# Kernel optimization log

Measured on AMD Instinct MI355X. Metric: run time of the kernel, lower is better.

The kernel has to match this reference:

```python
import jax, jax.numpy as jnp
import numpy as np

MASK_ATTENTION = 10000000000.0
PAD_IDX = 0


def setup_inputs() -> dict:
    key = jax.random.key(0)
    ks = jax.random.split(key, 12)
    S, T, B, H, V = 256, 64, 8, 768, 50257
    return {
        "encoder_out": jax.random.normal(ks[0], (S, B, H), dtype=jnp.float32),
        "decoder_state": jax.random.normal(ks[1], (T, B, H), dtype=jnp.float32),
        "src_ids": jax.random.randint(ks[2], (S, B), 0, V, dtype=jnp.int64),
        "tgt_embedding": jax.random.normal(ks[3], (T, B, H), dtype=jnp.float32),
        "W_attn": jax.random.normal(ks[4], (2 * H, H), dtype=jnp.float32) * 0.02,
        "b_attn": jax.random.normal(ks[5], (H,), dtype=jnp.float32) * 0.02,
        "v_attn": jax.random.normal(ks[6], (H,), dtype=jnp.float32) * 0.02,
        "b_v": jax.random.normal(ks[7], (1,), dtype=jnp.float32) * 0.02,
        "W_pgen": jax.random.normal(ks[8], (3 * H, 1), dtype=jnp.float32) * 0.02,
        "b_pgen": jax.random.normal(ks[9], (1,), dtype=jnp.float32) * 0.02,
        "W_gen": jax.random.normal(ks[10], (H, V), dtype=jnp.float32) * 0.02,
        "b_gen": jax.random.normal(ks[11], (V,), dtype=jnp.float32) * 0.02,
    }


def reference(encoder_out, decoder_state, src_ids, tgt_embedding,
              W_attn, b_attn, v_attn, b_v, W_pgen, b_pgen, W_gen, b_gen):
    # encoder_out: [S,B,H], decoder_state/tgt_embedding: [T,B,H], src_ids: [S,B]
    T, B, H = decoder_state.shape
    S = encoder_out.shape[0]
    # Split the cat+Linear into two projections (same math as Linear on concat)
    Wd, We = W_attn[:H], W_attn[H:]
    dec_proj = decoder_state @ Wd                     # [T,B,H]
    enc_proj = encoder_out @ We + b_attn              # [S,B,H]
    energy = jnp.tanh(dec_proj[:, None] + enc_proj[None])  # [T,S,B,H]
    attention = energy @ v_attn + b_v[0]              # [T,S,B]
    pad_mask = (src_ids == PAD_IDX)                   # [S,B]
    attn_dist = jnp.where(pad_mask[None], -MASK_ATTENTION, attention)
    attn_prob = jax.nn.softmax(attn_dist, axis=1)     # softmax over S: [T,S,B]
    ctx = jnp.einsum('tsb,sbh->tbh', attn_prob, encoder_out)  # [T,B,H]
    p_gen_input = jnp.concatenate((decoder_state, ctx, tgt_embedding), axis=2)
    p_gen = jax.nn.sigmoid(p_gen_input @ W_pgen + b_pgen)     # [T,B,1]
    vocab_prob = jax.nn.softmax(decoder_state @ W_gen + b_gen, axis=2)  # [T,B,V]
    vocab_prob_ = vocab_prob * p_gen
    attn_prob_ = jnp.transpose(attn_prob, (0, 2, 1)) * (1.0 - p_gen)    # [T,B,S]
    idx = jnp.broadcast_to(src_ids.T[None], (T, B, S))                  # [T,B,S]
    ti = jnp.arange(T)[:, None, None]
    bi = jnp.arange(B)[None, :, None]
    final_prob = vocab_prob_.at[ti, bi, idx].add(attn_prob_)
    return final_prob


if __name__ == "__main__":
    out = reference(**setup_inputs())
    print(out.shape)
```

## Files before the change

### kernel.cpp

```cpp
#include <hip/hip_runtime.h>
#include <stdint.h>

#define S_ 256
#define T_ 64
#define B_ 8
#define H_ 768
#define V_ 50257
#define R_ 512
#define VP_ 50304

typedef __attribute__((ext_vector_type(8))) short short8;
typedef __attribute__((ext_vector_type(4))) float float4v;

__device__ __forceinline__ float bf2f(unsigned short u) {
  union { unsigned int i; float f; } x; x.i = ((unsigned int)u) << 16; return x.f;
}
__device__ __forceinline__ short f2bf(float f) {
  union { float f; unsigned int i; } x; x.f = f;
  unsigned int u = x.i;
  unsigned int r = u + 0x7fffu + ((u >> 16) & 1u);
  return (short)(r >> 16);
}
__device__ __forceinline__ float tanh_fast(float x) {
  x = fminf(10.f, fmaxf(-10.f, x));
  float e = __expf(2.f * x);
  return (e - 1.f) * __builtin_amdgcn_rcpf(e + 1.f);
}
__device__ __forceinline__ void gload16(const short* g, short* l) {
  __builtin_amdgcn_global_load_lds(
      (const __attribute__((address_space(1))) unsigned int*)g,
      (__attribute__((address_space(3))) unsigned int*)l, 16, 0, 0);
}
__device__ __forceinline__ int swz(int r, int c) {
  return r * 64 + (c ^ ((r & 7) * 8));
}

__global__ __launch_bounds__(256) void cvt_kernel(const float* dec, const float* enc,
                                                  short* dec16, short* enc16, float* rowsums) {
  int i = blockIdx.x * 256 + threadIdx.x;
  if (i < R_) rowsums[i] = 0.f;
  const int nd = R_ * H_;
  if (i < nd) dec16[i] = f2bf(dec[i]);
  else        enc16[i - nd] = f2bf(enc[i - nd]);
}

__global__ __launch_bounds__(256) void twat_kernel(const float* in, short* out) {
  __shared__ float tile[64][65];
  int n0 = blockIdx.x * 64;
  int k0 = blockIdx.y * 64;
  int t = threadIdx.x;
  int c = t & 63, rsub = t >> 6;
#pragma unroll
  for (int i = 0; i < 16; ++i) {
    int r = i * 4 + rsub;
    tile[r][c] = in[(size_t)(k0 + r) * 768 + n0 + c];
  }
  __syncthreads();
#pragma unroll
  for (int i = 0; i < 16; ++i) {
    int nn = i * 4 + rsub;
    out[(size_t)(n0 + nn) * 1536 + k0 + c] = f2bf(tile[c][nn]);
  }
}

__global__ __launch_bounds__(256) void cvt_wt_kernel(const float* __restrict__ in,
                                                     short* __restrict__ out) {
  __shared__ float tile[64][65];
  int v0 = blockIdx.x * 64;
  int k0 = blockIdx.y * 64;
  int t = threadIdx.x;
  int c = t & 63, rsub = t >> 6;
#pragma unroll
  for (int i = 0; i < 16; ++i) {
    int r = i * 4 + rsub;
    int v = v0 + c;
    tile[r][c] = (v < V_) ? in[(size_t)(k0 + r) * V_ + v] : 0.f;
  }
  __syncthreads();
  int cp = t & 31, nsub = t >> 5;
#pragma unroll
  for (int i = 0; i < 8; ++i) {
    int nn = i * 8 + nsub;
    unsigned int pk = (unsigned int)(unsigned short)f2bf(tile[2 * cp][nn]) |
                      ((unsigned int)(unsigned short)f2bf(tile[2 * cp + 1][nn]) << 16);
    *(unsigned int*)&out[(size_t)(v0 + nn) * 768 + k0 + 2 * cp] = pk;
  }
}

__global__ __launch_bounds__(256) void gemm_proj(const short* __restrict__ A,
                                                 const short* __restrict__ BT,
                                                 int koff, const float* bias, float* C) {
  __shared__ short Al[128 * 32];
  __shared__ short Bl[64 * 32];
  int t = threadIdx.x;
  int w = t >> 6, l = t & 63;
  int m0 = blockIdx.y * 128, n0 = blockIdx.x * 64;
  int wm = w >> 1, wn = w & 1;
  float4v acc[4][2];
#pragma unroll
  for (int i = 0; i < 4; ++i)
#pragma unroll
    for (int j = 0; j < 2; ++j) acc[i][j] = float4v{0.f, 0.f, 0.f, 0.f};

#pragma unroll 1
  for (int kk = 0; kk < 768; kk += 32) {
#pragma unroll
    for (int i = 0; i < 2; ++i) {
      int q = t + i * 256;
      int m = q >> 2, k8 = (q & 3) * 8;
      *(short8*)&Al[m * 32 + k8] = *(const short8*)&A[(size_t)(m0 + m) * 768 + kk + k8];
    }
    {
      int n = t >> 2, k8 = (t & 3) * 8;
      *(short8*)&Bl[n * 32 + k8] = *(const short8*)&BT[(size_t)(n0 + n) * 1536 + koff + kk + k8];
    }
    __syncthreads();
    short8 af[4], bfr[2];
#pragma unroll
    for (int mt = 0; mt < 4; ++mt)
      af[mt] = *(short8*)&Al[(wm * 64 + mt * 16 + (l & 15)) * 32 + (l >> 4) * 8];
#pragma unroll
    for (int nt = 0; nt < 2; ++nt)
      bfr[nt] = *(short8*)&Bl[(wn * 32 + nt * 16 + (l & 15)) * 32 + (l >> 4) * 8];
#pragma unroll
    for (int mt = 0; mt < 4; ++mt)
#pragma unroll
      for (int nt = 0; nt < 2; ++nt)
        acc[mt][nt] = __builtin_amdgcn_mfma_f32_16x16x32_bf16(af[mt], bfr[nt], acc[mt][nt], 0, 0, 0);
    __syncthreads();
  }
  int q4 = (l >> 4) * 4, ln = l & 15;
#pragma unroll
  for (int nt = 0; nt < 2; ++nt) {
    int c = n0 + wn * 32 + nt * 16 + ln;
    float bv = bias ? bias[c] : 0.f;
#pragma unroll
    for (int mt = 0; mt < 4; ++mt)
#pragma unroll
      for (int r = 0; r < 4; ++r) {
        int row = m0 + wm * 64 + mt * 16 + q4 + r;
        C[(size_t)row * 768 + c] = acc[mt][nt][r] + bv;
      }
  }
}

__global__ __launch_bounds__(256) void energy_kernel(const float* __restrict__ dproj,
                                                     const float* __restrict__ eproj,
                                                     const float* vattn, const float* bv,
                                                     float* scores) {
  __shared__ float dch[16][65];
  __shared__ float ech[16][65];
  __shared__ float vch[64];
  int s0 = blockIdx.x * 16;
  int b  = blockIdx.y;
  int t0 = blockIdx.z * 16;
  int t = threadIdx.x;
  int sl = t & 15, tl = t >> 4;
  float acc = 0.f;
  for (int hc = 0; hc < 768; hc += 64) {
#pragma unroll
    for (int i = 0; i < 4; ++i) {
      int idx = i * 256 + t;
      int rr = idx >> 6, cc = idx & 63;
      dch[rr][cc] = dproj[(size_t)((t0 + rr) * 8 + b) * 768 + hc + cc];
      ech[rr][cc] = eproj[(size_t)((s0 + rr) * 8 + b) * 768 + hc + cc];
    }
    if (t < 64) vch[t] = vattn[hc + t];
    __syncthreads();
#pragma unroll 8
    for (int hh = 0; hh < 64; ++hh) {
      float x = dch[tl][hh] + ech[sl][hh];
      acc = fmaf(tanh_fast(x), vch[hh], acc);
    }
    __syncthreads();
  }
  scores[(size_t)((t0 + tl) * 8 + b) * 256 + s0 + sl] = acc + bv[0];
}

__global__ __launch_bounds__(256) void softmax_kernel(const float* scores, const int* sid, float* P) {
  __shared__ float red[256];
  int r = blockIdx.x, t = threadIdx.x, b = r & 7;
  float v = scores[(size_t)r * 256 + t];
  if (sid[t * 8 + b] == 0) v = -1e10f;
  red[t] = v;
  __syncthreads();
  for (int s = 128; s > 0; s >>= 1) {
    if (t < s) red[t] = fmaxf(red[t], red[t + s]);
    __syncthreads();
  }
  float m = red[0];
  __syncthreads();
  float e = __expf(v - m);
  red[t] = e;
  __syncthreads();
  for (int s = 128; s > 0; s >>= 1) {
    if (t < s) red[t] += red[t + s];
    __syncthreads();
  }
  P[(size_t)r * 256 + t] = e * (1.f / red[0]);
}

__global__ __launch_bounds__(256) void ctx_kernel(const float* __restrict__ P,
                                                  const float* __restrict__ enc, float* ctx) {
  __shared__ float Pl[16][256];
  int h0 = blockIdx.x * 64;
  int b  = blockIdx.y;
  int tg = blockIdx.z;
  int t = threadIdx.x;
  int hl = t & 63, wv = t >> 6;
#pragma unroll
  for (int i = 0; i < 16; ++i) {
    int idx = i * 256 + t;
    int tt = idx >> 8, s = idx & 255;
    Pl[tt][s] = P[(size_t)((tg * 16 + tt) * 8 + b) * 256 + s];
  }
  __syncthreads();
  float acc[4] = {0.f, 0.f, 0.f, 0.f};
#pragma unroll 4
  for (int s = 0; s < 256; ++s) {
    float e = enc[(size_t)(s * 8 + b) * 768 + h0 + hl];
#pragma unroll
    for (int j = 0; j < 4; ++j)
      acc[j] = fmaf(Pl[wv * 4 + j][s], e, acc[j]);
  }
#pragma unroll
  for (int j = 0; j < 4; ++j)
    ctx[(size_t)((tg * 16 + wv * 4 + j) * 8 + b) * 768 + h0 + hl] = acc[j];
}

__global__ __launch_bounds__(256) void pgen_kernel(const float* dec, const float* ctx,
                                                   const float* tgt, const float* Wp,
                                                   const float* bp, float* pgen) {
  __shared__ float red[256];
  int r = blockIdx.x, t = threadIdx.x;
  float s = 0.f;
  for (int h = t; h < 768; h += 256) {
    s = fmaf(dec[(size_t)r * 768 + h], Wp[h], s);
    s = fmaf(ctx[(size_t)r * 768 + h], Wp[768 + h], s);
    s = fmaf(tgt[(size_t)r * 768 + h], Wp[1536 + h], s);
  }
  red[t] = s;
  __syncthreads();
  for (int st = 128; st > 0; st >>= 1) {
    if (t < st) red[t] += red[t + st];
    __syncthreads();
  }
  if (t == 0) pgen[r] = 1.f / (1.f + __expf(-(red[0] + bp[0])));
}

__global__ __launch_bounds__(256, 3) void gemm_vocab(const short* __restrict__ A,
                                                     const short* __restrict__ BT,
                                                     const float* __restrict__ bgen,
                                                     short* __restrict__ E, float* rowsums) {
  __shared__ __align__(16) short Bl[2][128 * 64];
  int t = threadIdx.x;
  int w = t >> 6, l = t & 63;
  int orig = blockIdx.x;
  int xcd = orig & 7, ix = orig >> 3;
  int wgid = (xcd < 4 ? xcd * 197 : 788 + (xcd - 4) * 196) + ix;
  int n0 = (wgid >> 2) * 128;
  int m0 = (wgid & 3) * 128;
  int wm = w >> 1, wn = w & 1;
  int lm = l & 15, lq = l >> 4;
  int srow = t >> 3;
  int scol = ((t & 7) ^ (srow & 7)) * 8;

  float4v acc[4][4];
#pragma unroll
  for (int i = 0; i < 4; ++i)
#pragma unroll
    for (int j = 0; j < 4; ++j) acc[i][j] = float4v{0.f, 0.f, 0.f, 0.f};

  const short* bS = BT + (size_t)(n0 + srow) * 768 + scol;
  const short* aR = A + (size_t)(m0 + wm * 64 + lm) * 768 + lq * 8;

  auto STAGE = [&](int buf, int kk) {
#pragma unroll
    for (int i = 0; i < 4; ++i)
      gload16(bS + (size_t)i * 32 * 768 + kk, &Bl[buf][(i * 32 + w * 8) * 64]);
  };

  STAGE(0, 0);
#pragma unroll 1
  for (int kt = 0; kt < 12; ++kt) {
    int cb = kt & 1;
    int kk = kt * 64;
    short8 af[2][4];
#pragma unroll
    for (int ks = 0; ks < 2; ++ks)
#pragma unroll
      for (int mt = 0; mt < 4; ++mt)
        af[ks][mt] = *(const short8*)&aR[(size_t)mt * 16 * 768 + kk + ks * 32];
    if (kt < 11) {
      STAGE(cb ^ 1, kk + 64);
      asm volatile("s_waitcnt vmcnt(12)" ::: "memory");
    } else {
      asm volatile("s_waitcnt vmcnt(8)" ::: "memory");
    }
    __builtin_amdgcn_s_barrier();

    short8 bfr[2][4];
#pragma unroll
    for (int ks = 0; ks < 2; ++ks)
#pragma unroll
      for (int nt = 0; nt < 4; ++nt)
        bfr[ks][nt] = *(const short8*)&Bl[cb][swz(wn * 64 + nt * 16 + lm, ks * 32 + lq * 8)];
    asm volatile("s_waitcnt lgkmcnt(0)" ::: "memory");
    if (kt < 11)
      asm volatile("s_waitcnt vmcnt(4)" ::: "memory");
    else
      asm volatile("s_waitcnt vmcnt(0)" ::: "memory");
    __builtin_amdgcn_s_barrier();

#pragma unroll
    for (int ks = 0; ks < 2; ++ks)
#pragma unroll
      for (int mt = 0; mt < 4; ++mt)
#pragma unroll
        for (int nt = 0; nt < 4; ++nt)
          acc[mt][nt] = __builtin_amdgcn_mfma_f32_16x16x32_bf16(af[ks][mt], bfr[ks][nt],
                                                                acc[mt][nt], 0, 0, 0);
  }

  int q4 = lq * 4, ln = lm;
  float rs[4][4];
#pragma unroll
  for (int i = 0; i < 4; ++i)
#pragma unroll
    for (int j = 0; j < 4; ++j) rs[i][j] = 0.f;
#pragma unroll
  for (int nt = 0; nt < 4; ++nt) {
    int c = n0 + wn * 64 + nt * 16 + ln;
    bool valid = c < V_;
    float bg = valid ? bgen[c] : 0.f;
#pragma unroll
    for (int mt = 0; mt < 4; ++mt)
#pragma unroll
      for (int r = 0; r < 4; ++r) {
        float e = valid ? __expf(acc[mt][nt][r] + bg) : 0.f;
        int row = m0 + wm * 64 + mt * 16 + q4 + r;
        E[(size_t)row * VP_ + c] = f2bf(e);
        rs[mt][r] += e;
      }
  }
#pragma unroll
  for (int mt = 0; mt < 4; ++mt)
#pragma unroll
    for (int r = 0; r < 4; ++r) {
      float v = rs[mt][r];
      v += __shfl_xor(v, 1);
      v += __shfl_xor(v, 2);
      v += __shfl_xor(v, 4);
      v += __shfl_xor(v, 8);
      if (ln == 0) atomicAdd(&rowsums[m0 + wm * 64 + mt * 16 + q4 + r], v);
    }
}

__global__ __launch_bounds__(256) void final_kernel(const short* __restrict__ E,
                                                    const float* __restrict__ P,
                                                    const float* pgen, const float* rowsums,
                                                    const int* sid, float* __restrict__ out) {
  int r = blockIdx.y, t = threadIdx.x, b = r & 7;
  int lo = blockIdx.x * 2048, hi = lo + 2048;
  float pg = pgen[r];
  float scale = pg / rowsums[r];
  const short* Er = E + (size_t)r * VP_;
  float* outr = out + (size_t)r * V_;
  int c0 = lo + t * 8;
  if (c0 < V_) {
    short8 ev = *(const short8*)&Er[c0];
#pragma unroll
    for (int j = 0; j < 8; ++j) {
      int c = c0 + j;
      if (c < V_) outr[c] = bf2f((unsigned short)ev[j]) * scale;
    }
  }
  __syncthreads();
  int idx = sid[t * 8 + b];
  if (idx >= lo && idx < hi) {
    float ap = (1.f - pg) * P[(size_t)r * 256 + t];
    atomicAdd(&outr[idx], ap);
  }
}

extern "C" void kernel_launch(void* const* d_in, const int* in_sizes, int n_in,
                              void* d_out, int out_size, void* d_ws, size_t ws_size,
                              hipStream_t stream) {
  const float* enc  = (const float*)d_in[0];
  const float* dec  = (const float*)d_in[1];
  const int*   sid  = (const int*)d_in[2];
  const float* tgt  = (const float*)d_in[3];
  const float* Wat  = (const float*)d_in[4];
  const float* batt = (const float*)d_in[5];
  const float* vatt = (const float*)d_in[6];
  const float* bv   = (const float*)d_in[7];
  const float* Wp   = (const float*)d_in[8];
  const float* bp   = (const float*)d_in[9];
  const float* Wg   = (const float*)d_in[10];
  const float* bg   = (const float*)d_in[11];
  float* out = (float*)d_out;

  char* ws = (char*)d_ws;
  size_t off = 0;
  auto alloc = [&](size_t bytes) -> char* {
    char* p = ws + off;
    off += (bytes + 255) & ~(size_t)255;
    return p;
  };
  short* E16     = (short*)alloc((size_t)R_ * VP_ * 2);
  short* WT16    = (short*)alloc((size_t)VP_ * H_ * 2);
  short* dec16   = (short*)alloc((size_t)R_ * H_ * 2);
  short* enc16   = (short*)alloc((size_t)S_ * B_ * H_ * 2);
  short* WAT16   = (short*)alloc((size_t)H_ * 1536 * 2);
  float* dproj   = (float*)alloc((size_t)R_ * H_ * 4);
  float* eproj   = (float*)alloc((size_t)S_ * B_ * H_ * 4);
  float* scores  = (float*)alloc((size_t)R_ * 256 * 4);
  float* P       = (float*)alloc((size_t)R_ * 256 * 4);
  float* ctx     = (float*)alloc((size_t)R_ * H_ * 4);
  float* pgen    = (float*)alloc(R_ * 4);
  float* rowsums = (float*)alloc(R_ * 4);

  cvt_kernel<<<7680, 256, 0, stream>>>(dec, enc, dec16, enc16, rowsums);
  twat_kernel<<<dim3(12, 24), 256, 0, stream>>>(Wat, WAT16);
  cvt_wt_kernel<<<dim3(786, 12), 256, 0, stream>>>(Wg, WT16);
  gemm_proj<<<dim3(12, 4), 256, 0, stream>>>(dec16, WAT16, 0, nullptr, dproj);
  gemm_proj<<<dim3(12, 16), 256, 0, stream>>>(enc16, WAT16, 768, batt, eproj);
  energy_kernel<<<dim3(16, 8, 4), 256, 0, stream>>>(dproj, eproj, vatt, bv, scores);
  softmax_kernel<<<512, 256, 0, stream>>>(scores, sid, P);
  ctx_kernel<<<dim3(12, 8, 4), 256, 0, stream>>>(P, enc, ctx);
  pgen_kernel<<<512, 256, 0, stream>>>(dec, ctx, tgt, Wp, bp, pgen);
  gemm_vocab<<<dim3(1572), 256, 0, stream>>>(dec16, WT16, bg, E16, rowsums);
  final_kernel<<<dim3(25, 512), 256, 0, stream>>>(E16, P, pgen, rowsums, sid, out);
}
```

Before: 603.2 us.

## Rework projection GEMM, vectorize conversions, replace global rowsum atomics with two-stage reduce

```diff
diff --git a/kernel.cpp b/kernel.cpp
--- a/kernel.cpp
+++ b/kernel.cpp
@@ -8,6 +8,8 @@
 #define V_ 50257
 #define R_ 512
 #define VP_ 50304
+#define NBLK_ 393
+#define NBP_ 400
 
 typedef __attribute__((ext_vector_type(8))) short short8;
 typedef __attribute__((ext_vector_type(4))) float float4v;
@@ -22,9 +24,9 @@
   return (short)(r >> 16);
 }
 __device__ __forceinline__ float tanh_fast(float x) {
-  x = fminf(10.f, fmaxf(-10.f, x));
-  float e = __expf(2.f * x);
-  return (e - 1.f) * __builtin_amdgcn_rcpf(e + 1.f);
+  float e = __builtin_amdgcn_exp2f(2.885390082f * x);
+  float r = __builtin_amdgcn_rcpf(e + 1.f);
+  return fmaf(-2.f, r, 1.f);
 }
 __device__ __forceinline__ void gload16(const short* g, short* l) {
   __builtin_amdgcn_global_load_lds(
@@ -35,13 +37,22 @@
   return r * 64 + (c ^ ((r & 7) * 8));
 }
 
-__global__ __launch_bounds__(256) void cvt_kernel(const float* dec, const float* enc,
-                                                  short* dec16, short* enc16, float* rowsums) {
-  int i = blockIdx.x * 256 + threadIdx.x;
-  if (i < R_) rowsums[i] = 0.f;
-  const int nd = R_ * H_;
-  if (i < nd) dec16[i] = f2bf(dec[i]);
-  else        enc16[i - nd] = f2bf(enc[i - nd]);
+__global__ __launch_bounds__(256) void cvt_kernel(const float* __restrict__ dec,
+                                                  const float* __restrict__ enc,
+                                                  short* __restrict__ dec16,
+                                                  short* __restrict__ enc16, float* rowsums) {
+  int tid = blockIdx.x * 256 + threadIdx.x;
+  if (tid < R_) rowsums[tid] = 0.f;
+  const int nd4 = R_ * H_ / 4;
+  const float4v* src;
+  short* dst;
+  int off;
+  if (tid < nd4) { src = (const float4v*)dec; dst = dec16; off = tid; }
+  else           { src = (const float4v*)enc; dst = enc16; off = tid - nd4; }
+  float4v v = src[off];
+  union { short s[4]; unsigned long long u; } pk;
+  pk.s[0] = f2bf(v[0]); pk.s[1] = f2bf(v[1]); pk.s[2] = f2bf(v[2]); pk.s[3] = f2bf(v[3]);
+  *(unsigned long long*)&dst[(size_t)off * 4] = pk.u;
 }
 
 __global__ __launch_bounds__(256) void twat_kernel(const float* in, short* out) {
@@ -65,82 +76,110 @@
 
 __global__ __launch_bounds__(256) void cvt_wt_kernel(const float* __restrict__ in,
                                                      short* __restrict__ out) {
-  __shared__ float tile[64][65];
-  int v0 = blockIdx.x * 64;
+  __shared__ float tile[64][133];
+  int v0 = blockIdx.x * 128;
   int k0 = blockIdx.y * 64;
   int t = threadIdx.x;
-  int c = t & 63, rsub = t >> 6;
-#pragma unroll
-  for (int i = 0; i < 16; ++i) {
-    int r = i * 4 + rsub;
-    int v = v0 + c;
-    tile[r][c] = (v < V_) ? in[(size_t)(k0 + r) * V_ + v] : 0.f;
-  }
-  __syncthreads();
-  int cp = t & 31, nsub = t >> 5;
-#pragma unroll
-  for (int i = 0; i < 8; ++i) {
-    int nn = i * 8 + nsub;
-    unsigned int pk = (unsigned int)(unsigned short)f2bf(tile[2 * cp][nn]) |
-                      ((unsigned int)(unsigned short)f2bf(tile[2 * cp + 1][nn]) << 16);
-    *(unsigned int*)&out[(size_t)(v0 + nn) * 768 + k0 + 2 * cp] = pk;
-  }
-}
-
-__global__ __launch_bounds__(256) void gemm_proj(const short* __restrict__ A,
-                                                 const short* __restrict__ BT,
-                                                 int koff, const float* bias, float* C) {
-  __shared__ short Al[128 * 32];
-  __shared__ short Bl[64 * 32];
+  int lc = t & 127, lr2 = t >> 7;
+#pragma unroll
+  for (int p = 0; p < 32; ++p) {
+    int r = p * 2 + lr2;
+    int v = v0 + lc;
+    tile[r][lc] = (v < V_) ? in[(size_t)(k0 + r) * V_ + v] : 0.f;
+  }
+  __syncthreads();
+  int kg = t & 7, vsub = t >> 3;
+#pragma unroll
+  for (int p = 0; p < 4; ++p) {
+    int vv = p * 32 + vsub;
+    union { short s[8]; short8 v8; } pk;
+#pragma unroll
+    for (int j = 0; j < 8; ++j) pk.s[j] = f2bf(tile[kg * 8 + j][vv]);
+    *(short8*)&out[(size_t)(v0 + vv) * 768 + k0 + kg * 8] = pk.v8;
+  }
+}
+
+__global__ __launch_bounds__(256, 3) void gemm_proj(const short* __restrict__ A,
+                                                    const short* __restrict__ BT,
+                                                    int koff, const float* __restrict__ bias,
+                                                    float* __restrict__ C) {
+  __shared__ __align__(16) short Bl[2][128 * 64];
   int t = threadIdx.x;
   int w = t >> 6, l = t & 63;
-  int m0 = blockIdx.y * 128, n0 = blockIdx.x * 64;
+  int n0 = blockIdx.x * 128;
+  int m0 = blockIdx.y * 128;
   int wm = w >> 1, wn = w & 1;
-  float4v acc[4][2];
+  int lm = l & 15, lq = l >> 4;
+  int srow = t >> 3;
+  int scol = ((t & 7) ^ (srow & 7)) * 8;
+
+  float4v acc[4][4];
 #pragma unroll
   for (int i = 0; i < 4; ++i)
 #pragma unroll
-    for (int j = 0; j < 2; ++j) acc[i][j] = float4v{0.f, 0.f, 0.f, 0.f};
-
+    for (int j = 0; j < 4; ++j) acc[i][j] = float4v{0.f, 0.f, 0.f, 0.f};
+
+  const short* bS = BT + (size_t)(n0 + srow) * 1536 + koff + scol;
+  const short* aR = A + (size_t)(m0 + wm * 64 + lm) * 768 + lq * 8;
+
+  auto STAGE = [&](int buf, int kk) {
+#pragma unroll
+    for (int i = 0; i < 4; ++i)
+      gload16(bS + (size_t)i * 32 * 1536 + kk, &Bl[buf][(i * 32 + w * 8) * 64]);
+  };
+
+  STAGE(0, 0);
 #pragma unroll 1
-  for (int kk = 0; kk < 768; kk += 32) {
-#pragma unroll
-    for (int i = 0; i < 2; ++i) {
-      int q = t + i * 256;
-      int m = q >> 2, k8 = (q & 3) * 8;
-      *(short8*)&Al[m * 32 + k8] = *(const short8*)&A[(size_t)(m0 + m) * 768 + kk + k8];
+  for (int kt = 0; kt < 12; ++kt) {
+    int cb = kt & 1;
+    int kk = kt * 64;
+    short8 af[2][4];
+#pragma unroll
+    for (int ks = 0; ks < 2; ++ks)
+#pragma unroll
+      for (int mt = 0; mt < 4; ++mt)
+        af[ks][mt] = *(const short8*)&aR[(size_t)mt * 16 * 768 + kk + ks * 32];
+    if (kt < 11) {
+      STAGE(cb ^ 1, kk + 64);
+      asm volatile("s_waitcnt vmcnt(12)" ::: "memory");
+    } else {
+      asm volatile("s_waitcnt vmcnt(8)" ::: "memory");
     }
-    {
-      int n = t >> 2, k8 = (t & 3) * 8;
-      *(short8*)&Bl[n * 32 + k8] = *(const short8*)&BT[(size_t)(n0 + n) * 1536 + koff + kk + k8];
-    }
-    __syncthreads();
-    short8 af[4], bfr[2];
+    __builtin_amdgcn_s_barrier();
+
+    short8 bfr[2][4];
+#pragma unroll
+    for (int ks = 0; ks < 2; ++ks)
+#pragma unroll
+      for (int nt = 0; nt < 4; ++nt)
+        bfr[ks][nt] = *(const short8*)&Bl[cb][swz(wn * 64 + nt * 16 + lm, ks * 32 + lq * 8)];
+    asm volatile("s_waitcnt lgkmcnt(0)" ::: "memory");
+    if (kt < 11)
+      asm volatile("s_waitcnt vmcnt(4)" ::: "memory");
+    else
+      asm volatile("s_waitcnt vmcnt(0)" ::: "memory");
+    __builtin_amdgcn_s_barrier();
+
+#pragma unroll
+    for (int ks = 0; ks < 2; ++ks)
+#pragma unroll
+      for (int mt = 0; mt < 4; ++mt)
+#pragma unroll
+        for (int nt = 0; nt < 4; ++nt)
+          acc[mt][nt] = __builtin_amdgcn_mfma_f32_16x16x32_bf16(af[ks][mt], bfr[ks][nt],
+                                                                acc[mt][nt], 0, 0, 0);
+  }
+
+  int q4 = lq * 4, ln = lm;
+#pragma unroll
+  for (int nt = 0; nt < 4; ++nt) {
+    int c = n0 + wn * 64 + nt * 16 + ln;
+    float bv = bias ? bias[c] : 0.f;
 #pragma unroll
     for (int mt = 0; mt < 4; ++mt)
-      af[mt] = *(short8*)&Al[(wm * 64 + mt * 16 + (l & 15)) * 32 + (l >> 4) * 8];
-#pragma unroll
-    for (int nt = 0; nt < 2; ++nt)
-      bfr[nt] = *(short8*)&Bl[(wn * 32 + nt * 16 + (l & 15)) * 32 + (l >> 4) * 8];
-#pragma unroll
-    for (int mt = 0; mt < 4; ++mt)
-#pragma unroll
-      for (int nt = 0; nt < 2; ++nt)
-        acc[mt][nt] = __builtin_amdgcn_mfma_f32_16x16x32_bf16(af[mt], bfr[nt], acc[mt][nt], 0, 0, 0);
-    __syncthreads();
-  }
-  int q4 = (l >> 4) * 4, ln = l & 15;
-#pragma unroll
-  for (int nt = 0; nt < 2; ++nt) {
-    int c = n0 + wn * 32 + nt * 16 + ln;
-    float bv = bias ? bias[c] : 0.f;
-#pragma unroll
-    for (int mt = 0; mt < 4; ++mt)
-#pragma unroll
-      for (int r = 0; r < 4; ++r) {
-        int row = m0 + wm * 64 + mt * 16 + q4 + r;
-        C[(size_t)row * 768 + c] = acc[mt][nt][r] + bv;
-      }
+#pragma unroll
+      for (int r = 0; r < 4; ++r)
+        C[(size_t)(m0 + wm * 64 + mt * 16 + q4 + r) * 768 + c] = acc[mt][nt][r] + bv;
   }
 }
 
@@ -251,7 +290,8 @@
 __global__ __launch_bounds__(256, 3) void gemm_vocab(const short* __restrict__ A,
                                                      const short* __restrict__ BT,
                                                      const float* __restrict__ bgen,
-                                                     short* __restrict__ E, float* rowsums) {
+                                                     short* __restrict__ E,
+                                                     float* __restrict__ prs) {
   __shared__ __align__(16) short Bl[2][128 * 64];
   int t = threadIdx.x;
   int w = t >> 6, l = t & 63;
@@ -260,6 +300,7 @@
   int wgid = (xcd < 4 ? xcd * 197 : 788 + (xcd - 4) * 196) + ix;
   int n0 = (wgid >> 2) * 128;
   int m0 = (wgid & 3) * 128;
+  int nblk = wgid >> 2;
   int wm = w >> 1, wn = w & 1;
   int lm = l & 15, lq = l >> 4;
   int srow = t >> 3;
@@ -343,6 +384,9 @@
         rs[mt][r] += e;
       }
   }
+  float* red = (float*)Bl;
+  if (t < 128) red[t] = 0.f;
+  __syncthreads();
 #pragma unroll
   for (int mt = 0; mt < 4; ++mt)
 #pragma unroll
@@ -352,8 +396,25 @@
       v += __shfl_xor(v, 2);
       v += __shfl_xor(v, 4);
       v += __shfl_xor(v, 8);
-      if (ln == 0) atomicAdd(&rowsums[m0 + wm * 64 + mt * 16 + q4 + r], v);
+      if (ln == 0) atomicAdd(&red[wm * 64 + mt * 16 + q4 + r], v);
     }
+  __syncthreads();
+  if (t < 128) prs[(size_t)(m0 + t) * NBP_ + nblk] = red[t];
+}
+
+__global__ __launch_bounds__(256) void rowsum_reduce(const float* __restrict__ prs,
+                                                     float* __restrict__ rowsums) {
+  __shared__ float red[256];
+  int r = blockIdx.x, t = threadIdx.x;
+  float s = prs[(size_t)r * NBP_ + t];
+  if (t + 256 < NBLK_) s += prs[(size_t)r * NBP_ + t + 256];
+  red[t] = s;
+  __syncthreads();
+  for (int st = 128; st > 0; st >>= 1) {
+    if (t < st) red[t] += red[t + st];
+    __syncthreads();
+  }
+  if (t == 0) rowsums[r] = red[0];
 }
 
 __global__ __launch_bounds__(256) void final_kernel(const short* __restrict__ E,
@@ -366,14 +427,10 @@
   float scale = pg / rowsums[r];
   const short* Er = E + (size_t)r * VP_;
   float* outr = out + (size_t)r * V_;
-  int c0 = lo + t * 8;
-  if (c0 < V_) {
-    short8 ev = *(const short8*)&Er[c0];
-#pragma unroll
-    for (int j = 0; j < 8; ++j) {
-      int c = c0 + j;
-      if (c < V_) outr[c] = bf2f((unsigned short)ev[j]) * scale;
-    }
+#pragma unroll
+  for (int j = 0; j < 8; ++j) {
+    int c = lo + j * 256 + t;
+    if (c < V_) outr[c] = bf2f((unsigned short)Er[c]) * scale;
   }
   __syncthreads();
   int idx = sid[t * 8 + b];
@@ -419,16 +476,18 @@
   float* ctx     = (float*)alloc((size_t)R_ * H_ * 4);
   float* pgen    = (float*)alloc(R_ * 4);
   float* rowsums = (float*)alloc(R_ * 4);
-
-  cvt_kernel<<<7680, 256, 0, stream>>>(dec, enc, dec16, enc16, rowsums);
+  float* prs     = (float*)alloc((size_t)R_ * NBP_ * 4);
+
+  cvt_kernel<<<1920, 256, 0, stream>>>(dec, enc, dec16, enc16, rowsums);
   twat_kernel<<<dim3(12, 24), 256, 0, stream>>>(Wat, WAT16);
-  cvt_wt_kernel<<<dim3(786, 12), 256, 0, stream>>>(Wg, WT16);
-  gemm_proj<<<dim3(12, 4), 256, 0, stream>>>(dec16, WAT16, 0, nullptr, dproj);
-  gemm_proj<<<dim3(12, 16), 256, 0, stream>>>(enc16, WAT16, 768, batt, eproj);
+  cvt_wt_kernel<<<dim3(393, 12), 256, 0, stream>>>(Wg, WT16);
+  gemm_proj<<<dim3(6, 4), 256, 0, stream>>>(dec16, WAT16, 0, nullptr, dproj);
+  gemm_proj<<<dim3(6, 16), 256, 0, stream>>>(enc16, WAT16, 768, batt, eproj);
   energy_kernel<<<dim3(16, 8, 4), 256, 0, stream>>>(dproj, eproj, vatt, bv, scores);
   softmax_kernel<<<512, 256, 0, stream>>>(scores, sid, P);
   ctx_kernel<<<dim3(12, 8, 4), 256, 0, stream>>>(P, enc, ctx);
   pgen_kernel<<<512, 256, 0, stream>>>(dec, ctx, tgt, Wp, bp, pgen);
-  gemm_vocab<<<dim3(1572), 256, 0, stream>>>(dec16, WT16, bg, E16, rowsums);
+  gemm_vocab<<<dim3(1572), 256, 0, stream>>>(dec16, WT16, bg, E16, prs);
+  rowsum_reduce<<<512, 256, 0, stream>>>(prs, rowsums);
   final_kernel<<<dim3(25, 512), 256, 0, stream>>>(E16, P, pgen, rowsums, sid, out);
 }
```

New measurement: 586.2 us. 2.8% less time.
